# Performance work log

Hardware: AMD Instinct MI355X
Metric: run time of the kernel (lower is better)

The kernel has to match this reference:

```python
import jax, jax.numpy as jnp
import numpy as np

N_STEPS = 8  # DGL GatedGraphConv n_steps as hardcoded in GatedGCN.__init__


def _gru(a, h, Wih, Whh, bih, bhh):
    # torch.nn.GRUCell: gate order (r, z, n)
    gi = a @ Wih.T + bih          # [N, 3d]
    gh = h @ Whh.T + bhh          # [N, 3d]
    ir, iz, inn = jnp.split(gi, 3, axis=-1)
    hr, hz, hn = jnp.split(gh, 3, axis=-1)
    r = jax.nn.sigmoid(ir + hr)
    z = jax.nn.sigmoid(iz + hz)
    n = jnp.tanh(inn + r * hn)
    return (1.0 - z) * n + z * h


def _gated_conv(h, src, dst, W, b, Wih, Whh, bih, bhh):
    # DGL GatedGraphConv with a single etype: for each step,
    # message = Linear(h[src]); aggregate = sum over in-edges; h = GRU(agg, h)
    N = h.shape[0]

    def step(h, _):
        m = h @ W.T + b                                   # [N, d] linear per node (message fn)
        agg = jax.ops.segment_sum(m[src], dst, num_segments=N)  # [N, d] sum over in-edges
        return _gru(agg, h, Wih, Whh, bih, bhh), None

    h, _ = jax.lax.scan(step, h, None, length=N_STEPS)
    return h


def setup_inputs() -> dict:
    key = jax.random.key(0)
    ks = jax.random.split(key, 10)
    N, E, D = 50000, 800000, 128  # in_feats = h_feats = num_classes = 128
    s = 1.0 / np.sqrt(D)
    return {
        "in_feat": jax.random.normal(ks[0], (N, D), jnp.float32),
        "src": jax.random.randint(ks[1], (E,), 0, N),
        "dst": jax.random.randint(ks[2], (E,), 0, N),
        "W1": jax.random.normal(ks[3], (D, D), jnp.float32) * s,
        "b1": jnp.zeros((D,), jnp.float32),
        "Wih1": jax.random.normal(ks[4], (3 * D, D), jnp.float32) * s,
        "Whh1": jax.random.normal(ks[5], (3 * D, D), jnp.float32) * s,
        "bih1": jnp.zeros((3 * D,), jnp.float32),
        "bhh1": jnp.zeros((3 * D,), jnp.float32),
        "W2": jax.random.normal(ks[6], (D, D), jnp.float32) * s,
        "b2": jnp.zeros((D,), jnp.float32),
        "Wih2": jax.random.normal(ks[7], (3 * D, D), jnp.float32) * s,
        "Whh2": jax.random.normal(ks[8], (3 * D, D), jnp.float32) * s,
        "bih2": jnp.zeros((3 * D,), jnp.float32),
        "bhh2": jnp.zeros((3 * D,), jnp.float32),
    }


def reference(in_feat, src, dst, W1, b1, Wih1, Whh1, bih1, bhh1,
              W2, b2, Wih2, Whh2, bih2, bhh2):
    # in_feats == h_feats so DGL's zero-padding of the input is a no-op here.
    h = _gated_conv(in_feat, src, dst, W1, b1, Wih1, Whh1, bih1, bhh1)
    h = jax.nn.relu(h)
    h = _gated_conv(h, src, dst, W2, b2, Wih2, Whh2, bih2, bhh2)
    # dgl.mean_nodes with a single graph -> [1, num_classes]
    return jnp.mean(h, axis=0, keepdims=True)
```

## Files before the change

kernel.cpp:

```cpp
#include <hip/hip_runtime.h>
#include <hip/hip_bf16.h>
#include <cmath>

#define DD 128

typedef __attribute__((ext_vector_type(8))) short short8v;
typedef __attribute__((ext_vector_type(4))) float floatx4;

__device__ __forceinline__ float sigmoid_f(float x) { return 1.0f / (1.0f + __expf(-x)); }
__device__ __forceinline__ float tanh_f(float x) {
  float e = __expf(2.0f * x);
  return 1.0f - 2.0f / (e + 1.0f);
}
__device__ __forceinline__ unsigned short f2bf(float x) {
  __hip_bfloat16 b = __float2bfloat16(x);
  return *reinterpret_cast<unsigned short*>(&b);
}
__device__ __forceinline__ float bf2f(unsigned short s) {
  return __uint_as_float(((unsigned int)s) << 16);
}

__global__ __launch_bounds__(256) void deg_count(const int* __restrict__ dst,
                                                 int* __restrict__ deg, int E) {
  int e = blockIdx.x * blockDim.x + threadIdx.x;
  if (e < E) atomicAdd(&deg[dst[e]], 1);
}

__global__ __launch_bounds__(256) void scan_part(const int* __restrict__ deg,
                                                 int* __restrict__ bsum, int N) {
  __shared__ int s[256];
  int tid = threadIdx.x;
  int i = blockIdx.x * 256 + tid;
  s[tid] = (i < N) ? deg[i] : 0;
  __syncthreads();
  for (int st = 128; st > 0; st >>= 1) {
    if (tid < st) s[tid] += s[tid + st];
    __syncthreads();
  }
  if (tid == 0) bsum[blockIdx.x] = s[0];
}

__global__ __launch_bounds__(256) void scan_top(const int* __restrict__ bsum,
                                                int* __restrict__ bofs, int nb) {
  __shared__ int s[256];
  int tid = threadIdx.x;
  int v = (tid < nb) ? bsum[tid] : 0;
  s[tid] = v;
  __syncthreads();
  for (int o = 1; o < 256; o <<= 1) {
    int t = (tid >= o) ? s[tid - o] : 0;
    __syncthreads();
    s[tid] += t;
    __syncthreads();
  }
  if (tid < nb) bofs[tid] = s[tid] - v;
  if (tid == nb - 1) bofs[nb] = s[tid];
}

__global__ __launch_bounds__(256) void scan_final(const int* __restrict__ deg,
                                                  const int* __restrict__ bofs,
                                                  int* __restrict__ ofs,
                                                  int* __restrict__ cur, int N) {
  __shared__ int s[256];
  int tid = threadIdx.x;
  int i = blockIdx.x * 256 + tid;
  int v = (i < N) ? deg[i] : 0;
  s[tid] = v;
  __syncthreads();
  for (int o = 1; o < 256; o <<= 1) {
    int t = (tid >= o) ? s[tid - o] : 0;
    __syncthreads();
    s[tid] += t;
    __syncthreads();
  }
  int off = bofs[blockIdx.x] + s[tid] - v;
  if (i < N) {
    ofs[i] = off;
    cur[i] = off;
    if (i == N - 1) ofs[N] = off + v;
  }
}

__global__ __launch_bounds__(256) void fill_csr(const int* __restrict__ src,
                                                const int* __restrict__ dst,
                                                int* __restrict__ cur,
                                                int* __restrict__ eidx, int E) {
  int e = blockIdx.x * blockDim.x + threadIdx.x;
  if (e < E) {
    int p = atomicAdd(&cur[dst[e]], 1);
    eidx[p] = src[e];
  }
}

__global__ __launch_bounds__(128) void fuse_w(const float* __restrict__ Wih,
                                              const float* __restrict__ W,
                                              float* __restrict__ Wc32) {
  int r = blockIdx.x;
  int k = threadIdx.x;
  float acc = 0.0f;
  for (int j = 0; j < DD; ++j) acc = fmaf(Wih[r * DD + j], W[j * DD + k], acc);
  Wc32[(size_t)r * DD + k] = acc;
}

__global__ __launch_bounds__(128) void fuse_u(const float* __restrict__ Wih,
                                              const float* __restrict__ b,
                                              float* __restrict__ u) {
  int r = blockIdx.x * 128 + threadIdx.x;
  if (r < 3 * DD) {
    float acc = 0.0f;
    for (int j = 0; j < DD; ++j) acc = fmaf(Wih[r * DD + j], b[j], acc);
    u[r] = acc;
  }
}

__global__ __launch_bounds__(256) void split_w(const float* __restrict__ Wf,
                                               const float* __restrict__ Whh,
                                               unsigned short* __restrict__ Wp) {
  int i = blockIdx.x * 256 + threadIdx.x;
  const int TOT = 6 * DD * DD;
  if (i < TOT) {
    int r = i >> 7;
    float x = (r < 3 * DD) ? Wf[i] : Whh[i - 3 * DD * DD];
    unsigned short hb = f2bf(x);
    float xr = x - bf2f(hb);
    unsigned short mb = f2bf(xr);
    float x2 = xr - bf2f(mb);
    unsigned short lb = f2bf(x2);
    Wp[i] = hb;
    Wp[TOT + i] = mb;
    Wp[2 * TOT + i] = lb;
  }
}

__global__ __launch_bounds__(256) void gather_h(const float* __restrict__ h,
                                                const int* __restrict__ ofs,
                                                const int* __restrict__ eidx,
                                                float* __restrict__ agg, int N) {
  int node = blockIdx.x * 8 + (threadIdx.x >> 5);
  if (node >= N) return;
  int l = (threadIdx.x & 31) << 2;
  int beg = ofs[node], end = ofs[node + 1];
  float4 a0 = {0.f, 0.f, 0.f, 0.f}, a1 = {0.f, 0.f, 0.f, 0.f};
  float4 a2 = {0.f, 0.f, 0.f, 0.f}, a3 = {0.f, 0.f, 0.f, 0.f};
  int e = beg;
  for (; e + 3 < end; e += 4) {
    int s0 = eidx[e], s1 = eidx[e + 1], s2 = eidx[e + 2], s3 = eidx[e + 3];
    float4 v0 = *(const float4*)(h + (size_t)s0 * DD + l);
    float4 v1 = *(const float4*)(h + (size_t)s1 * DD + l);
    float4 v2 = *(const float4*)(h + (size_t)s2 * DD + l);
    float4 v3 = *(const float4*)(h + (size_t)s3 * DD + l);
    a0.x += v0.x; a0.y += v0.y; a0.z += v0.z; a0.w += v0.w;
    a1.x += v1.x; a1.y += v1.y; a1.z += v1.z; a1.w += v1.w;
    a2.x += v2.x; a2.y += v2.y; a2.z += v2.z; a2.w += v2.w;
    a3.x += v3.x; a3.y += v3.y; a3.z += v3.z; a3.w += v3.w;
  }
  for (; e + 1 < end; e += 2) {
    int s0 = eidx[e], s1 = eidx[e + 1];
    float4 v0 = *(const float4*)(h + (size_t)s0 * DD + l);
    float4 v1 = *(const float4*)(h + (size_t)s1 * DD + l);
    a0.x += v0.x; a0.y += v0.y; a0.z += v0.z; a0.w += v0.w;
    a1.x += v1.x; a1.y += v1.y; a1.z += v1.z; a1.w += v1.w;
  }
  if (e < end) {
    float4 v = *(const float4*)(h + (size_t)eidx[e] * DD + l);
    a0.x += v.x; a0.y += v.y; a0.z += v.z; a0.w += v.w;
  }
  float4 r;
  r.x = (a0.x + a1.x) + (a2.x + a3.x);
  r.y = (a0.y + a1.y) + (a2.y + a3.y);
  r.z = (a0.z + a1.z) + (a2.z + a3.z);
  r.w = (a0.w + a1.w) + (a2.w + a3.w);
  *(float4*)(agg + (size_t)node * DD + l) = r;
}

__device__ __forceinline__ void split8(const float* p, short8v& q0, short8v& q1, short8v& q2) {
  float4 v0 = *(const float4*)(p);
  float4 v1 = *(const float4*)(p + 4);
  float f[8] = {v0.x, v0.y, v0.z, v0.w, v1.x, v1.y, v1.z, v1.w};
#pragma unroll
  for (int e = 0; e < 8; ++e) {
    float x = f[e];
    unsigned short hb = f2bf(x);
    float xr = x - bf2f(hb);
    unsigned short mb = f2bf(xr);
    float x2 = xr - bf2f(mb);
    q0[e] = (short)hb;
    q1[e] = (short)mb;
    q2[e] = (short)f2bf(x2);
  }
}

__global__ __launch_bounds__(256, 2) void gru_mfma3(
    const float* __restrict__ Agg, const float* __restrict__ H,
    const unsigned short* __restrict__ Wp,
    const float* __restrict__ bih, const float* __restrict__ bhh,
    const float* __restrict__ u, const int* __restrict__ deg,
    float* __restrict__ Hout, int N, int do_relu)
{
  __shared__ short sB[2][96 * DD];
  const int TOT = 6 * DD * DD;
  const int tid = threadIdx.x;
  const int wid = tid >> 6;
  const int lane = tid & 63;
  const int lrow = lane & 15;
  const int hi = lane >> 4;
  const int lk = hi * 8;
  const int rowBase = blockIdx.x * 128 + wid * 32;
  const int j0 = blockIdx.y * 32;

  floatx4 acc[6][2][2];
#pragma unroll
  for (int g = 0; g < 6; ++g)
#pragma unroll
    for (int ct = 0; ct < 2; ++ct)
#pragma unroll
      for (int rt = 0; rt < 2; ++rt) acc[g][ct][rt] = (floatx4){0.f, 0.f, 0.f, 0.f};

  int r0 = rowBase + lrow;       if (r0 >= N) r0 = N - 1;
  int r1 = rowBase + 16 + lrow;  if (r1 >= N) r1 = N - 1;

  int s_row[6], s_cnk[6];
  size_t s_grow[6];
#pragma unroll
  for (int i = 0; i < 6; ++i) {
    int ch = tid + i * 256;
    s_row[i] = ch >> 4;
    s_cnk[i] = ch & 15;
    s_grow[i] = (size_t)((s_row[i] >> 5) * DD + j0 + (s_row[i] & 31));
  }

  short8v wreg[12];
#pragma unroll
  for (int i = 0; i < 6; ++i) {
    wreg[i]     = *(const short8v*)(Wp + 0 * TOT + s_grow[i] * DD + s_cnk[i] * 8);
    wreg[6 + i] = *(const short8v*)(Wp + 1 * TOT + s_grow[i] * DD + s_cnk[i] * 8);
  }

  short8v frag[3][4][2];
#pragma unroll
  for (int kc = 0; kc < 4; ++kc) {
    split8(Agg + (size_t)r0 * DD + kc * 32 + lk, frag[0][kc][0], frag[1][kc][0], frag[2][kc][0]);
    split8(Agg + (size_t)r1 * DD + kc * 32 + lk, frag[0][kc][1], frag[1][kc][1], frag[2][kc][1]);
  }

#pragma unroll
  for (int arr = 0; arr < 2; ++arr) {
    const size_t gbase = (size_t)arr * 384 * DD;
    if (arr > 0) __syncthreads();
#pragma unroll
    for (int i = 0; i < 6; ++i) {
      int off = s_row[i] * DD + (s_cnk[i] ^ (s_row[i] & 7)) * 8;
      *(short8v*)(&sB[0][off]) = wreg[i];
      *(short8v*)(&sB[1][off]) = wreg[6 + i];
    }
#pragma unroll
    for (int i = 0; i < 6; ++i)
      wreg[i] = *(const short8v*)(Wp + 2 * TOT + gbase + s_grow[i] * DD + s_cnk[i] * 8);
    __syncthreads();

#pragma unroll
    for (int kc = 0; kc < 4; ++kc) {
#pragma unroll
      for (int gl = 0; gl < 3; ++gl) {
#pragma unroll
        for (int ct = 0; ct < 2; ++ct) {
          int lr = gl * 32 + ct * 16 + lrow;
          int off = lr * DD + ((kc * 4 + hi) ^ (lr & 7)) * 8;
          short8v bh = *(const short8v*)(&sB[0][off]);
#pragma unroll
          for (int rt = 0; rt < 2; ++rt) {
            acc[arr * 3 + gl][ct][rt] = __builtin_amdgcn_mfma_f32_16x16x32_bf16(
                frag[0][kc][rt], bh, acc[arr * 3 + gl][ct][rt], 0, 0, 0);
            acc[arr * 3 + gl][ct][rt] = __builtin_amdgcn_mfma_f32_16x16x32_bf16(
                frag[1][kc][rt], bh, acc[arr * 3 + gl][ct][rt], 0, 0, 0);
            acc[arr * 3 + gl][ct][rt] = __builtin_amdgcn_mfma_f32_16x16x32_bf16(
                frag[2][kc][rt], bh, acc[arr * 3 + gl][ct][rt], 0, 0, 0);
          }
          short8v bm = *(const short8v*)(&sB[1][off]);
#pragma unroll
          for (int rt = 0; rt < 2; ++rt) {
            acc[arr * 3 + gl][ct][rt] = __builtin_amdgcn_mfma_f32_16x16x32_bf16(
                frag[0][kc][rt], bm, acc[arr * 3 + gl][ct][rt], 0, 0, 0);
            acc[arr * 3 + gl][ct][rt] = __builtin_amdgcn_mfma_f32_16x16x32_bf16(
                frag[1][kc][rt], bm, acc[arr * 3 + gl][ct][rt], 0, 0, 0);
          }
        }
      }
    }
    __syncthreads();

#pragma unroll
    for (int i = 0; i < 6; ++i) {
      int off = s_row[i] * DD + (s_cnk[i] ^ (s_row[i] & 7)) * 8;
      *(short8v*)(&sB[0][off]) = wreg[i];
    }
    if (arr == 0) {
      const size_t g1 = (size_t)384 * DD;
#pragma unroll
      for (int i = 0; i < 6; ++i) {
        wreg[i]     = *(const short8v*)(Wp + 0 * TOT + g1 + s_grow[i] * DD + s_cnk[i] * 8);
        wreg[6 + i] = *(const short8v*)(Wp + 1 * TOT + g1 + s_grow[i] * DD + s_cnk[i] * 8);
      }
    }
    __syncthreads();

#pragma unroll
    for (int kc = 0; kc < 4; ++kc) {
#pragma unroll
      for (int gl = 0; gl < 3; ++gl) {
#pragma unroll
        for (int ct = 0; ct < 2; ++ct) {
          int lr = gl * 32 + ct * 16 + lrow;
          int off = lr * DD + ((kc * 4 + hi) ^ (lr & 7)) * 8;
          short8v bl = *(const short8v*)(&sB[0][off]);
#pragma unroll
          for (int rt = 0; rt < 2; ++rt) {
            acc[arr * 3 + gl][ct][rt] = __builtin_amdgcn_mfma_f32_16x16x32_bf16(
                frag[0][kc][rt], bl, acc[arr * 3 + gl][ct][rt], 0, 0, 0);
          }
        }
      }
    }

    if (arr == 0) {
#pragma unroll
      for (int kc = 0; kc < 4; ++kc) {
        split8(H + (size_t)r0 * DD + kc * 32 + lk, frag[0][kc][0], frag[1][kc][0], frag[2][kc][0]);
        split8(H + (size_t)r1 * DD + kc * 32 + lk, frag[0][kc][1], frag[1][kc][1], frag[2][kc][1]);
      }
    }
  }

  float bi_r[2], bi_z[2], bi_n[2], bh_r[2], bh_z[2], bh_n[2], u_r[2], u_z[2], u_n[2];
#pragma unroll
  for (int ct = 0; ct < 2; ++ct) {
    int c = j0 + ct * 16 + lrow;
    bi_r[ct] = bih[c];  bi_z[ct] = bih[DD + c];  bi_n[ct] = bih[2 * DD + c];
    bh_r[ct] = bhh[c];  bh_z[ct] = bhh[DD + c];  bh_n[ct] = bhh[2 * DD + c];
    u_r[ct]  = u[c];    u_z[ct]  = u[DD + c];    u_n[ct]  = u[2 * DD + c];
  }

#pragma unroll
  for (int rt = 0; rt < 2; ++rt) {
#pragma unroll
    for (int q = 0; q < 4; ++q) {
      int row = rowBase + rt * 16 + hi * 4 + q;
      if (row < N) {
        float dg = (float)deg[row];
#pragma unroll
        for (int ct = 0; ct < 2; ++ct) {
          int c = j0 + ct * 16 + lrow;
          float ir = acc[0][ct][rt][q] + bi_r[ct] + dg * u_r[ct];
          float iz = acc[1][ct][rt][q] + bi_z[ct] + dg * u_z[ct];
          float in = acc[2][ct][rt][q] + bi_n[ct] + dg * u_n[ct];
          float hr = acc[3][ct][rt][q] + bh_r[ct];
          float hz = acc[4][ct][rt][q] + bh_z[ct];
          float hn = acc[5][ct][rt][q] + bh_n[ct];
          float rg = sigmoid_f(ir + hr);
          float zg = sigmoid_f(iz + hz);
          float ng = tanh_f(in + rg * hn);
          float hold = H[(size_t)row * DD + c];
          float out = (1.0f - zg) * ng + zg * hold;
          if (do_relu) out = fmaxf(out, 0.0f);
          Hout[(size_t)row * DD + c] = out;
        }
      }
    }
  }
}

__global__ __launch_bounds__(256) void col_mean(
    const float* __restrict__ H, float* __restrict__ out, int N)
{
  __shared__ float s[256];
  int c = threadIdx.x & 127;
  int rg = threadIdx.x >> 7;
  float acc = 0.0f;
  for (int r = blockIdx.x * 2 + rg; r < N; r += gridDim.x * 2)
    acc += H[(size_t)r * DD + c];
  s[threadIdx.x] = acc;
  __syncthreads();
  if (threadIdx.x < 128) {
    float v = (s[threadIdx.x] + s[threadIdx.x + 128]) * (1.0f / (float)N);
    unsafeAtomicAdd(out + c, v);
  }
}

extern "C" void kernel_launch(void* const* d_in, const int* in_sizes, int n_in,
                              void* d_out, int out_size, void* d_ws, size_t ws_size,
                              hipStream_t stream) {
  const float* in_feat = (const float*)d_in[0];
  const int* src = (const int*)d_in[1];
  const int* dst = (const int*)d_in[2];
  const float* W[2]   = {(const float*)d_in[3], (const float*)d_in[9]};
  const float* bb[2]  = {(const float*)d_in[4], (const float*)d_in[10]};
  const float* Wih[2] = {(const float*)d_in[5], (const float*)d_in[11]};
  const float* Whh[2] = {(const float*)d_in[6], (const float*)d_in[12]};
  const float* bih[2] = {(const float*)d_in[7], (const float*)d_in[13]};
  const float* bhh[2] = {(const float*)d_in[8], (const float*)d_in[14]};
  const int N = in_sizes[0] / DD;
  const int E = in_sizes[1];

  const size_t nd = (size_t)N * DD;
  char* base = (char*)d_ws;
  float* hA  = (float*)base; base += nd * sizeof(float);
  float* hB  = (float*)base; base += nd * sizeof(float);
  float* agg = (float*)base; base += nd * sizeof(float);
  float* Wc32 = (float*)base; base += (size_t)3 * DD * DD * sizeof(float);
  unsigned short* Wp[2];
  Wp[0] = (unsigned short*)base; base += (size_t)3 * 6 * DD * DD * sizeof(unsigned short);
  Wp[1] = (unsigned short*)base; base += (size_t)3 * 6 * DD * DD * sizeof(unsigned short);
  float* u[2];
  u[0] = (float*)base; base += 3 * DD * sizeof(float);
  u[1] = (float*)base; base += 3 * DD * sizeof(float);
  int* deg  = (int*)base; base += (size_t)N * sizeof(int);
  int* ofs  = (int*)base; base += ((size_t)N + 1) * sizeof(int);
  int* cur  = (int*)base; base += (size_t)N * sizeof(int);
  int* eidx = (int*)base; base += (size_t)E * sizeof(int);
  int* bsum = (int*)base; base += 256 * sizeof(int);
  int* bofs = (int*)base; base += 257 * sizeof(int);

  const int nb = (N + 255) / 256;

  hipMemsetAsync(deg, 0, (size_t)N * sizeof(int), stream);
  deg_count<<<(E + 255) / 256, 256, 0, stream>>>(dst, deg, E);
  scan_part<<<nb, 256, 0, stream>>>(deg, bsum, N);
  scan_top<<<1, 256, 0, stream>>>(bsum, bofs, nb);
  scan_final<<<nb, 256, 0, stream>>>(deg, bofs, ofs, cur, N);
  fill_csr<<<(E + 255) / 256, 256, 0, stream>>>(src, dst, cur, eidx, E);

  for (int layer = 0; layer < 2; ++layer) {
    fuse_w<<<3 * DD, 128, 0, stream>>>(Wih[layer], W[layer], Wc32);
    split_w<<<(6 * DD * DD + 255) / 256, 256, 0, stream>>>(Wc32, Whh[layer], Wp[layer]);
    fuse_u<<<3, 128, 0, stream>>>(Wih[layer], bb[layer], u[layer]);
  }

  hipMemcpyAsync(hA, in_feat, nd * sizeof(float), hipMemcpyDeviceToDevice, stream);

  float* hcur = hA;
  float* hnxt = hB;
  const int gblocks = (N + 7) / 8;
  const int mblocks = (N + 127) / 128;

  for (int layer = 0; layer < 2; ++layer) {
    for (int step_i = 0; step_i < 8; ++step_i) {
      gather_h<<<gblocks, 256, 0, stream>>>(hcur, ofs, eidx, agg, N);
      int do_relu = (layer == 0 && step_i == 7) ? 1 : 0;
      gru_mfma3<<<dim3(mblocks, 4), 256, 0, stream>>>(
          agg, hcur, Wp[layer], bih[layer], bhh[layer],
          u[layer], deg, hnxt, N, do_relu);
      float* t = hcur; hcur = hnxt; hnxt = t;
    }
  }

  hipMemsetAsync(d_out, 0, DD * sizeof(float), stream);
  col_mean<<<256, 256, 0, stream>>>(hcur, (float*)d_out, N);
}
```

Measured before the change: 2.220 ms.

## Unroll gather by 8, raise GRU occupancy hint, remap GRU blocks for L2 locality

The gather kernel now issues eight independent row loads per iteration instead of four, so more memory requests are in flight. The GRU MFMA kernel's launch bound goes from 2 to 3 blocks per SM, which tightens the register budget and may cause spills. The 2D grid becomes a 1D grid with a swizzle that groups 8 row-blocks across the 4 column-blocks, so blocks reading the same rows run close together and share L2. The grid is padded to a multiple of 8 row-blocks and relies on the existing row clamp to handle the extra blocks.

```diff
diff --git a/kernel.cpp b/kernel.cpp
--- a/kernel.cpp
+++ b/kernel.cpp
@@ -140,36 +140,36 @@
   if (node >= N) return;
   int l = (threadIdx.x & 31) << 2;
   int beg = ofs[node], end = ofs[node + 1];
-  float4 a0 = {0.f, 0.f, 0.f, 0.f}, a1 = {0.f, 0.f, 0.f, 0.f};
-  float4 a2 = {0.f, 0.f, 0.f, 0.f}, a3 = {0.f, 0.f, 0.f, 0.f};
+  float4 aa[4];
+#pragma unroll
+  for (int j = 0; j < 4; ++j) aa[j] = (float4){0.f, 0.f, 0.f, 0.f};
   int e = beg;
-  for (; e + 3 < end; e += 4) {
-    int s0 = eidx[e], s1 = eidx[e + 1], s2 = eidx[e + 2], s3 = eidx[e + 3];
-    float4 v0 = *(const float4*)(h + (size_t)s0 * DD + l);
-    float4 v1 = *(const float4*)(h + (size_t)s1 * DD + l);
-    float4 v2 = *(const float4*)(h + (size_t)s2 * DD + l);
-    float4 v3 = *(const float4*)(h + (size_t)s3 * DD + l);
-    a0.x += v0.x; a0.y += v0.y; a0.z += v0.z; a0.w += v0.w;
-    a1.x += v1.x; a1.y += v1.y; a1.z += v1.z; a1.w += v1.w;
-    a2.x += v2.x; a2.y += v2.y; a2.z += v2.z; a2.w += v2.w;
-    a3.x += v3.x; a3.y += v3.y; a3.z += v3.z; a3.w += v3.w;
+  for (; e + 7 < end; e += 8) {
+    float4 v[8];
+#pragma unroll
+    for (int j = 0; j < 8; ++j)
+      v[j] = *(const float4*)(h + (size_t)eidx[e + j] * DD + l);
+#pragma unroll
+    for (int j = 0; j < 8; ++j) {
+      aa[j & 3].x += v[j].x; aa[j & 3].y += v[j].y;
+      aa[j & 3].z += v[j].z; aa[j & 3].w += v[j].w;
+    }
   }
   for (; e + 1 < end; e += 2) {
-    int s0 = eidx[e], s1 = eidx[e + 1];
-    float4 v0 = *(const float4*)(h + (size_t)s0 * DD + l);
-    float4 v1 = *(const float4*)(h + (size_t)s1 * DD + l);
-    a0.x += v0.x; a0.y += v0.y; a0.z += v0.z; a0.w += v0.w;
-    a1.x += v1.x; a1.y += v1.y; a1.z += v1.z; a1.w += v1.w;
+    float4 v0 = *(const float4*)(h + (size_t)eidx[e] * DD + l);
+    float4 v1 = *(const float4*)(h + (size_t)eidx[e + 1] * DD + l);
+    aa[0].x += v0.x; aa[0].y += v0.y; aa[0].z += v0.z; aa[0].w += v0.w;
+    aa[1].x += v1.x; aa[1].y += v1.y; aa[1].z += v1.z; aa[1].w += v1.w;
   }
   if (e < end) {
     float4 v = *(const float4*)(h + (size_t)eidx[e] * DD + l);
-    a0.x += v.x; a0.y += v.y; a0.z += v.z; a0.w += v.w;
+    aa[0].x += v.x; aa[0].y += v.y; aa[0].z += v.z; aa[0].w += v.w;
   }
   float4 r;
-  r.x = (a0.x + a1.x) + (a2.x + a3.x);
-  r.y = (a0.y + a1.y) + (a2.y + a3.y);
-  r.z = (a0.z + a1.z) + (a2.z + a3.z);
-  r.w = (a0.w + a1.w) + (a2.w + a3.w);
+  r.x = (aa[0].x + aa[1].x) + (aa[2].x + aa[3].x);
+  r.y = (aa[0].y + aa[1].y) + (aa[2].y + aa[3].y);
+  r.z = (aa[0].z + aa[1].z) + (aa[2].z + aa[3].z);
+  r.w = (aa[0].w + aa[1].w) + (aa[2].w + aa[3].w);
   *(float4*)(agg + (size_t)node * DD + l) = r;
 }
 
@@ -190,7 +190,7 @@
   }
 }
 
-__global__ __launch_bounds__(256, 2) void gru_mfma3(
+__global__ __launch_bounds__(256, 3) void gru_mfma3(
     const float* __restrict__ Agg, const float* __restrict__ H,
     const unsigned short* __restrict__ Wp,
     const float* __restrict__ bih, const float* __restrict__ bhh,
@@ -205,8 +205,13 @@
   const int lrow = lane & 15;
   const int hi = lane >> 4;
   const int lk = hi * 8;
-  const int rowBase = blockIdx.x * 128 + wid * 32;
-  const int j0 = blockIdx.y * 32;
+
+  const int bid = blockIdx.x;
+  const int m = bid >> 5;
+  const int jb = (bid >> 3) & 3;
+  const int mb = (m << 3) | (bid & 7);
+  const int rowBase = mb * 128 + wid * 32;
+  const int j0 = jb * 32;
 
   floatx4 acc[6][2][2];
 #pragma unroll
@@ -441,12 +446,14 @@
   float* hnxt = hB;
   const int gblocks = (N + 7) / 8;
   const int mblocks = (N + 127) / 128;
+  const int mbP = (mblocks + 7) & ~7;
+  const int gruBlocks = mbP * 4;
 
   for (int layer = 0; layer < 2; ++layer) {
     for (int step_i = 0; step_i < 8; ++step_i) {
       gather_h<<<gblocks, 256, 0, stream>>>(hcur, ofs, eidx, agg, N);
       int do_relu = (layer == 0 && step_i == 7) ? 1 : 0;
-      gru_mfma3<<<dim3(mblocks, 4), 256, 0, stream>>>(
+      gru_mfma3<<<gruBlocks, 256, 0, stream>>>(
           agg, hcur, Wp[layer], bih[layer], bhh[layer],
           u[layer], deg, hnxt, N, do_relu);
       float* t = hcur; hcur = hnxt; hnxt = t;
```

Result: slower. 2.508 ms (+13.0%).
